# Kernel tuning notes

Hardware: AMD Instinct MI355X
Metric: run time of the kernel (lower is better)

Reference implementation:

```python
import jax, jax.numpy as jnp
import numpy as np

VOCAB = 23      # prime -> all nonzero scales invertible mod VOCAB
LEN = 256
BATCH = 512
HIDDEN = 4096
TEMP = 0.1


def _inv_table(v):
    # multiplicative inverse table mod v; inv(0) := 0 (non-invertible element)
    return np.array([0] + [pow(a, -1, v) for a in range(1, v)], dtype=np.int32)


def st_one_hot_argmax(x, temperature):
    """Straight-through one-hot argmax with tempered-softmax gradient."""
    soft = jax.nn.softmax(x / temperature, axis=-1)
    hard = jax.nn.one_hot(jnp.argmax(x, axis=-1), x.shape[-1], dtype=x.dtype)
    return soft + jax.lax.stop_gradient(hard - soft)


def one_hot_minus(inputs, shift):
    """(inputs - shift) % V in one-hot space via circular convolution."""
    V = inputs.shape[-1]
    # shift_matrix[..., u, v] = shift[..., (v - u) % V]  (== roll(shift, u))
    idx = (jnp.arange(V)[None, :] - jnp.arange(V)[:, None]) % V  # [u, v]
    shift_matrix = shift[..., idx]                               # [..., u, v]
    return jnp.einsum('...v,...uv->...u', inputs, shift_matrix)


def one_hot_multiply(inputs, scale):
    """(inputs * scale) % V in one-hot space; scale=0 component is dropped."""
    V = inputs.shape[-1]
    perm = (jnp.arange(V)[:, None] * jnp.arange(V)[None, :]) % V  # [a, v]
    P = jax.nn.one_hot(perm, V, dtype=inputs.dtype)               # [a, v, u]
    scale0 = scale * (jnp.arange(V) != 0).astype(scale.dtype)     # zero a=0 row
    return jnp.einsum('...v,...a,avu->...u', inputs, scale0, P)


def multiplicative_inverse(scale, v):
    """One-hot multiplicative inverse mod v via constant lookup table."""
    Inv = jax.nn.one_hot(jnp.asarray(_inv_table(v)), v, dtype=scale.dtype)  # [a, u]
    return jnp.einsum('...a,au->...u', scale, Inv)


def setup_inputs() -> dict:
    key = jax.random.key(0)
    k1, k2, k3 = jax.random.split(key, 3)
    tokens = jax.random.randint(k1, (BATCH, LEN), 0, VOCAB)
    inputs = jax.nn.one_hot(tokens, VOCAB, dtype=jnp.float32)     # [B, L, V]
    mask = (jnp.arange(LEN) % 2).astype(jnp.float32)[:, None]     # [L, 1]
    s1 = 1.0 / np.sqrt(LEN * VOCAB)
    s2 = 1.0 / np.sqrt(HIDDEN)
    W1 = jax.random.normal(k2, (LEN * VOCAB, HIDDEN), dtype=jnp.float32) * s1
    b1 = jnp.zeros((HIDDEN,), dtype=jnp.float32)
    W2 = jax.random.normal(k3, (HIDDEN, LEN * 2 * VOCAB), dtype=jnp.float32) * s2
    b2 = jnp.zeros((LEN * 2 * VOCAB,), dtype=jnp.float32)
    return {"inputs": inputs, "mask": mask, "W1": W1, "b1": b1, "W2": W2, "b2": b2}


def reference(inputs, mask, W1, b1, W2, b2):
    B, L, V = inputs.shape
    masked_inputs = mask * inputs                                 # [B, L, V]
    # layer(mask * inputs): flatten -> MLP -> [B, L, 2V]
    h = jax.nn.relu(masked_inputs.reshape(B, L * V) @ W1 + b1)
    net = (h @ W2 + b2).reshape(B, L, 2 * V)
    loc, scale = net[..., :V], net[..., V:]
    loc = st_one_hot_argmax(loc, TEMP)
    scale = st_one_hot_argmax(scale, TEMP)
    inv_scale = multiplicative_inverse(scale, V)
    shifted = one_hot_minus(inputs, loc)
    masked_outputs = (1.0 - mask) * one_hot_multiply(shifted, inv_scale)
    return masked_inputs + masked_outputs
```

## Files before the change

kernel.cpp:

```cpp
#include <hip/hip_runtime.h>
#include <cstddef>
#include <cstdint>

#define VOC 23
#define SEQ 256
#define NB  512
#define HID 4096
#define NCOL 11776
#define NPK 5888
#define KP  12288
#define EPS_TIE 4e-5f

__constant__ int INV23[VOC] = {0,1,12,8,6,14,4,10,3,18,7,21,2,16,5,20,13,19,9,17,15,11,22};

typedef __attribute__((ext_vector_type(8))) short short8;
typedef __attribute__((ext_vector_type(4))) float f32x4;

static __device__ __forceinline__ unsigned int f2bf(float f) {
  unsigned int x = __float_as_uint(f);
  return (x + 0x7fffu + ((x >> 16) & 1u)) >> 16;
}
static __device__ __forceinline__ float bf2f(unsigned int u) {
  return __uint_as_float(u << 16);
}

#define GL2LDS(g, l) __builtin_amdgcn_global_load_lds(                      \
    (const __attribute__((address_space(1))) unsigned int*)(g),             \
    (__attribute__((address_space(3))) unsigned int*)(l), 16, 0, 0)

__global__ __launch_bounds__(256) void k_tok_copy(const float* __restrict__ in,
                                                  float* __restrict__ out,
                                                  int* __restrict__ tok) {
  const int b = blockIdx.x;
  const int l = threadIdx.x;
  const float* row = in + ((size_t)b * SEQ + l) * VOC;
  int t = 0; float best = -1.0f;
#pragma unroll
  for (int v = 0; v < VOC; ++v) { float x = row[v]; if (x > best) { best = x; t = v; } }
  tok[b * SEQ + l] = t;
  if (l & 1) {
    float* o = out + ((size_t)b * SEQ + l) * VOC;
#pragma unroll
    for (int v = 0; v < VOC; ++v) o[v] = row[v];
  }
}

__global__ __launch_bounds__(256) void k_pack_w2(const float* __restrict__ W2,
                                                 unsigned short* __restrict__ Bp) {
  const int k0 = blockIdx.x * 64;
  const int j0 = blockIdx.y * 64;
  const int tid = threadIdx.x;
  __shared__ float T[64 * 65];
#pragma unroll
  for (int it = 0; it < 16; ++it) {
    int idx = it * 256 + tid;
    int k_l = idx >> 6, j_l = idx & 63;
    int j = j0 + j_l;
    int ee = j / 46, cc = j - ee * 46;
    T[j_l * 65 + k_l] = W2[(size_t)(k0 + k_l) * NCOL + 92 * ee + cc];
  }
  __syncthreads();
  const int j_l = tid >> 2, qt = tid & 3;
  unsigned int d[24];
#pragma unroll
  for (int pr = 0; pr < 8; ++pr) {
    int k_l = qt * 16 + pr * 2;
    float va = T[j_l * 65 + k_l], vb = T[j_l * 65 + k_l + 1];
    unsigned int ha = f2bf(va), la = f2bf(va - bf2f(ha));
    unsigned int hb = f2bf(vb), lb = f2bf(vb - bf2f(hb));
    d[pr * 3 + 0] = ha | (la << 16);
    d[pr * 3 + 1] = ha | (hb << 16);
    d[pr * 3 + 2] = lb | (hb << 16);
  }
  char* dst = ((char*)Bp) + (size_t)(j0 + j_l) * (KP * 2) + 6 * k0 + 96 * qt;
#pragma unroll
  for (int u = 0; u < 6; ++u) {
    uint4 w = make_uint4(d[4 * u], d[4 * u + 1], d[4 * u + 2], d[4 * u + 3]);
    ((uint4*)dst)[u] = w;
  }
}

__global__ __launch_bounds__(256) void k_hidden(const float* __restrict__ W1,
                                                const float* __restrict__ b1,
                                                const int* __restrict__ tok,
                                                float* __restrict__ h,
                                                unsigned short* __restrict__ Ap) {
  const int b = blockIdx.x;
  const int tid = threadIdx.x;
  __shared__ int rowS[128];
  if (tid < 128) {
    const int l = 2 * tid + 1;
    rowS[tid] = l * VOC + tok[b * SEQ + l];
  }
  __syncthreads();
  float4 acc[4];
#pragma unroll
  for (int j = 0; j < 4; ++j) acc[j] = make_float4(0.f, 0.f, 0.f, 0.f);
  for (int i = 0; i < 128; i += 2) {
    const float4* wr0 = (const float4*)(W1 + (size_t)rowS[i] * HID);
    const float4* wr1 = (const float4*)(W1 + (size_t)rowS[i + 1] * HID);
    float4 w0[4], w1[4];
#pragma unroll
    for (int j = 0; j < 4; ++j) w0[j] = wr0[tid + 256 * j];
#pragma unroll
    for (int j = 0; j < 4; ++j) w1[j] = wr1[tid + 256 * j];
#pragma unroll
    for (int j = 0; j < 4; ++j) {
      acc[j].x += w0[j].x; acc[j].y += w0[j].y; acc[j].z += w0[j].z; acc[j].w += w0[j].w;
      acc[j].x += w1[j].x; acc[j].y += w1[j].y; acc[j].z += w1[j].z; acc[j].w += w1[j].w;
    }
  }
  float4* hb = (float4*)(h + (size_t)b * HID);
  const float4* bv = (const float4*)b1;
#pragma unroll
  for (int j = 0; j < 4; ++j) {
    float4 bb = bv[tid + 256 * j];
    float4 r;
    r.x = fmaxf(acc[j].x + bb.x, 0.f);
    r.y = fmaxf(acc[j].y + bb.y, 0.f);
    r.z = fmaxf(acc[j].z + bb.z, 0.f);
    r.w = fmaxf(acc[j].w + bb.w, 0.f);
    hb[tid + 256 * j] = r;
    unsigned int h0 = f2bf(r.x), L0 = f2bf(r.x - bf2f(h0));
    unsigned int h1 = f2bf(r.y), L1 = f2bf(r.y - bf2f(h1));
    unsigned int h2 = f2bf(r.z), L2 = f2bf(r.z - bf2f(h2));
    unsigned int h3 = f2bf(r.w), L3 = f2bf(r.w - bf2f(h3));
    uint2* ap = (uint2*)(((char*)Ap) + (size_t)b * (KP * 2) + 24 * (tid + 256 * j));
    ap[0] = make_uint2(h0 | (h0 << 16), L0 | (h1 << 16));
    ap[1] = make_uint2(h1 | (L1 << 16), h2 | (h2 << 16));
    ap[2] = make_uint2(L2 | (h3 << 16), h3 | (L3 << 16));
  }
}

#define STAGE(bufA, bufB, kbv) do {                                               \
    _Pragma("unroll")                                                             \
    for (int c_ = 0; c_ < 2; ++c_) {                                              \
      GL2LDS(((const char*)Ap) + aG[c_] + (kbv), ((char*)(bufA)) + ldsOff[c_]);   \
      GL2LDS(((const char*)Bp) + bG[c_] + (kbv), ((char*)(bufB)) + ldsOff[c_]);   \
    }                                                                             \
  } while (0)

#define COMPUTE(bufA, bufB) do {                                                  \
    short8 a_[4], b_[4];                                                          \
    _Pragma("unroll")                                                             \
    for (int i_ = 0; i_ < 4; ++i_)                                                \
      a_[i_] = *(const short8*)((const char*)(bufA) + aoff + 1024 * i_);          \
    _Pragma("unroll")                                                             \
    for (int j_ = 0; j_ < 4; ++j_)                                                \
      b_[j_] = *(const short8*)((const char*)(bufB) + boff + 1024 * j_);          \
    _Pragma("unroll")                                                             \
    for (int i_ = 0; i_ < 4; ++i_)                                                \
      _Pragma("unroll")                                                           \
      for (int j_ = 0; j_ < 4; ++j_)                                              \
        acc[i_][j_] = __builtin_amdgcn_mfma_f32_16x16x32_bf16(a_[i_], b_[j_],     \
                                                              acc[i_][j_], 0, 0, 0); \
  } while (0)

__global__ __launch_bounds__(256) void k3_mfma(const unsigned short* __restrict__ Ap,
                                               const unsigned short* __restrict__ Bp,
                                               float* __restrict__ partial) {
  __shared__ unsigned short AsmD[2][128 * 32];
  __shared__ unsigned short BsmD[2][128 * 32];
  const int tid = threadIdx.x;

  const int f = blockIdx.x;
  const int nf = (f & 7) * 92 + (f >> 3);
  const int bn0 = (nf >> 4) * 128;
  const int inner = nf & 15;
  const int bm0 = (inner & 3) * 128;
  const int s = inner >> 2;

  const int lane = tid & 63, wave = tid >> 6;
  const int wm = wave & 1, wn = wave >> 1;
  const int r = lane & 15, q = lane >> 4;

  size_t aG[2], bG[2]; int ldsOff[2];
#pragma unroll
  for (int c = 0; c < 2; ++c) {
    const int G = c * 256 + tid;
    const int line = G >> 3, gph = G & 7;
    const int gin = gph ^ (line & 7);
    const int grow = 2 * line + (gin >> 2);
    const int gcol = (gin & 3) << 4;
    aG[c] = (size_t)(bm0 + grow) * (KP * 2) + gcol;
    bG[c] = (size_t)(bn0 + grow) * (KP * 2) + gcol;
    ldsOff[c] = G * 16;
  }

  const int gphR = (((((r & 1) << 2) | q) ^ ((r >> 1) & 7)) << 4);
  const int aoff = (32 * wm + (r >> 1)) * 128 + gphR;
  const int boff = (32 * wn + (r >> 1)) * 128 + gphR;

  f32x4 acc[4][4];
#pragma unroll
  for (int i = 0; i < 4; ++i)
#pragma unroll
    for (int j = 0; j < 4; ++j) acc[i][j] = (f32x4){0.f, 0.f, 0.f, 0.f};

  const int kb0 = s * 6144;
  STAGE(AsmD[0], BsmD[0], kb0);
  __syncthreads();
#pragma unroll 1
  for (int it = 0; it < 96; it += 2) {
    const int kb = kb0 + it * 64;
    STAGE(AsmD[1], BsmD[1], kb + 64);
    COMPUTE(AsmD[0], BsmD[0]);
    __syncthreads();
    if (it < 94) STAGE(AsmD[0], BsmD[0], kb + 128);
    COMPUTE(AsmD[1], BsmD[1]);
    __syncthreads();
  }

  float* pbase = partial + (size_t)s * NB * NPK;
#pragma unroll
  for (int i = 0; i < 4; ++i) {
    const int m = bm0 + 64 * wm + 16 * i + 4 * q;
#pragma unroll
    for (int j = 0; j < 4; ++j) {
      const int n = bn0 + 64 * wn + 16 * j + r;
      float* pp = pbase + (size_t)m * NPK + n;
#pragma unroll
      for (int reg = 0; reg < 4; ++reg)
        pp[(size_t)reg * NPK] = acc[i][j][reg];
    }
  }
}

__global__ __launch_bounds__(256) void k_epilogue(const float* __restrict__ partial,
                                                  const float* __restrict__ b2,
                                                  const int* __restrict__ tok,
                                                  int* __restrict__ win,
                                                  int* __restrict__ gcnt,
                                                  int* __restrict__ glist,
                                                  float* __restrict__ out) {
  const int b = blockIdx.x, tid = threadIdx.x;
  const int e = tid >> 1, grp = tid & 1;
  __shared__ int winS[256];
  __shared__ int flagS[256];
  float x[VOC];
  const size_t base = (size_t)b * NPK + 46 * e + 23 * grp;
#pragma unroll
  for (int c = 0; c < VOC; ++c) x[c] = b2[92 * e + 23 * grp + c];
#pragma unroll
  for (int s2 = 0; s2 < 4; ++s2) {
    const float* pp = partial + (size_t)s2 * NB * NPK + base;
#pragma unroll
    for (int c = 0; c < VOC; ++c) x[c] += pp[c];
  }
  float b0 = -1e30f, b1v = -1e30f; int bi = 0;
#pragma unroll
  for (int c = 0; c < VOC; ++c) {
    if (x[c] > b0) { b1v = b0; b0 = x[c]; bi = c; }
    else if (x[c] > b1v) b1v = x[c];
  }
  winS[tid] = bi;
  flagS[tid] = (b0 - b1v < EPS_TIE) ? 1 : 0;
  __syncthreads();
  if (!grp) {
    const int loc = winS[tid], sc = winS[tid + 1];
    win[b * 256 + 2 * e] = loc;
    win[b * 256 + 2 * e + 1] = sc;
    const int f0 = flagS[tid], f1 = flagS[tid + 1];
    if (f0 | f1) {
      int idx = atomicAdd(gcnt, 1);
      glist[idx] = e | (b << 7) | (f0 << 16) | (f1 << 17);
    }
    const int l = 2 * e;
    float* o = out + ((size_t)b * SEQ + l) * VOC;
    if (sc == 0) {
      for (int v = 0; v < VOC; ++v) o[v] = 0.f;
    } else {
      const int t = tok[b * SEQ + l];
      int dd = t - loc; if (dd < 0) dd += VOC;
      const int u = (INV23[sc] * dd) % VOC;
      for (int v = 0; v < VOC; ++v) o[v] = (v == u) ? 1.f : 0.f;
    }
  }
}

__global__ __launch_bounds__(192) void k_recheck(const float* __restrict__ h,
                                                 const float* __restrict__ W2,
                                                 const float* __restrict__ b2,
                                                 const int* __restrict__ tok,
                                                 const int* __restrict__ win,
                                                 const int* __restrict__ gcnt,
                                                 const int* __restrict__ glist,
                                                 float* __restrict__ out) {
  const int tid = threadIdx.x;
  __shared__ double dpart[184];
  __shared__ double dlog[VOC];
  __shared__ int decS[2];
  const int n = gcnt[0];
  for (int ei = blockIdx.x; ei < n; ei += 128) {
    const int ent = glist[ei];
    const int e = ent & 127, b = (ent >> 7) & 511;
    const int l = 2 * e;
#pragma unroll
    for (int grp = 0; grp < 2; ++grp) {
      if (!(ent & (1 << (16 + grp)))) {
        if (tid == 0) decS[grp] = win[b * 256 + 2 * e + grp];
      } else {
        const int col0 = 92 * e + 23 * grp;
        if (tid < 184) {
          const int c = tid >> 3, part = tid & 7;
          const float* hb = h + (size_t)b * HID;
          const size_t colc = (size_t)(col0 + c);
          double sacc[8] = {0, 0, 0, 0, 0, 0, 0, 0};
          const int kbase = part * 512;
          for (int kk = 0; kk < 512; kk += 8) {
#pragma unroll
            for (int t2 = 0; t2 < 8; ++t2) {
              const int k = kbase + kk + t2;
              sacc[t2] += (double)hb[k] * (double)W2[(size_t)k * NCOL + colc];
            }
          }
          dpart[tid] = ((sacc[0] + sacc[1]) + (sacc[2] + sacc[3])) +
                       ((sacc[4] + sacc[5]) + (sacc[6] + sacc[7]));
        }
        __syncthreads();
        if (tid < VOC) {
          double sd = (double)b2[col0 + tid];
#pragma unroll
          for (int p2 = 0; p2 < 8; ++p2) sd += dpart[tid * 8 + p2];
          dlog[tid] = sd;
        }
        __syncthreads();
        if (tid == 0) {
          double best = -1e300; int bi2 = 0;
#pragma unroll
          for (int c = 0; c < VOC; ++c)
            if (dlog[c] > best) { best = dlog[c]; bi2 = c; }
          decS[grp] = bi2;
        }
      }
      __syncthreads();
    }
    if (tid < VOC) {
      const int loc = decS[0], sc = decS[1];
      float val = 0.f;
      if (sc != 0) {
        const int t = tok[b * SEQ + l];
        int dd = t - loc; if (dd < 0) dd += VOC;
        const int u = (INV23[sc] * dd) % VOC;
        val = (tid == u) ? 1.f : 0.f;
      }
      out[((size_t)b * SEQ + l) * VOC + tid] = val;
    }
    __syncthreads();
  }
}

extern "C" void kernel_launch(void* const* d_in, const int* in_sizes, int n_in,
                              void* d_out, int out_size, void* d_ws, size_t ws_size,
                              hipStream_t stream) {
  const float* in  = (const float*)d_in[0];
  const float* W1  = (const float*)d_in[2];
  const float* b1  = (const float*)d_in[3];
  const float* W2  = (const float*)d_in[4];
  const float* b2  = (const float*)d_in[5];
  float* out = (float*)d_out;

  char* w = (char*)d_ws;
  int* tok = (int*)w;                         w += (size_t)NB * SEQ * 4;
  float* h = (float*)w;                       w += (size_t)NB * HID * 4;
  unsigned short* Ap = (unsigned short*)w;    w += (size_t)NB * KP * 2;
  unsigned short* Bp = (unsigned short*)w;    w += (size_t)NPK * KP * 2;
  float* partial = (float*)w;                 w += (size_t)4 * NB * NPK * 4;
  int* win = (int*)w;                         w += (size_t)NB * 256 * 4;
  int* gcnt = (int*)w;                        w += 256;
  int* glist = (int*)w;                       w += (size_t)65536 * 4;

  k_tok_copy<<<dim3(NB), dim3(256), 0, stream>>>(in, out, tok);
  k_pack_w2<<<dim3(64, 92), dim3(256), 0, stream>>>(W2, Bp);
  k_hidden<<<dim3(NB), dim3(256), 0, stream>>>(W1, b1, tok, h, Ap);
  hipMemsetAsync(gcnt, 0, 4, stream);
  k3_mfma<<<dim3(736), dim3(256), 0, stream>>>(Ap, Bp, partial);
  k_epilogue<<<dim3(NB), dim3(256), 0, stream>>>(partial, b2, tok, win, gcnt, glist, out);
  k_recheck<<<dim3(128), dim3(192), 0, stream>>>(h, W2, b2, tok, win, gcnt, glist, out);
}
```

Baseline: 699.8 us.

## Enlarge GEMM tiles to 256x256 with a 4-slot LDS async-load pipeline

Rewrites the main bf16 MFMA GEMM so each 512-thread block computes a 256x256 tile (8x4 MFMA fragments per wave) instead of 128x128. The K loop now streams into a 4-slot LDS ring buffer with three stages in flight, gated by explicit vmcnt waits and a single barrier per step. The setprio hint is raised around the MFMA bursts. The aim is more data reuse per LDS load and better hiding of global-memory latency. The cost is higher register pressure, 128KB of LDS per block, and only 184 blocks, which may underfill the CUs.

```diff
diff --git a/kernel.cpp b/kernel.cpp
--- a/kernel.cpp
+++ b/kernel.cpp
@@ -132,98 +132,132 @@
   }
 }
 
-#define STAGE(bufA, bufB, kbv) do {                                               \
+__global__ __launch_bounds__(512, 2) void k3_mfma(const unsigned short* __restrict__ Ap,
+                                                  const unsigned short* __restrict__ Bp,
+                                                  float* __restrict__ partial) {
+  __shared__ char lds3[4 * 32768];
+  const int tid = threadIdx.x;
+
+  const int f = blockIdx.x;
+  const int d = (f & 7) * 23 + (f >> 3);
+  const int g = d >> 1, mi = d & 1;
+  const int s = g / 23, n = g - s * 23;
+  const int bm0 = mi * 256;
+  const int bn0 = n * 256;
+  const int kb0 = s * 6144;
+
+  const int lane = tid & 63, wave = tid >> 6;
+  const int wm = wave & 1, wn = wave >> 1;
+  const int r = lane & 15, q = lane >> 4;
+
+  size_t gsrc[4]; int gdst[4];
+#pragma unroll
+  for (int c = 0; c < 4; ++c) {
+    const int G = (c & 1) * 512 + tid;
+    const int line = G >> 3, gph = G & 7;
+    const int gin = gph ^ (line & 7);
+    const int grow = 2 * line + (gin >> 2);
+    const int gcol = (gin & 3) << 4;
+    const int row0 = (c < 2 ? bm0 : bn0) + grow;
+    gsrc[c] = (size_t)row0 * (KP * 2) + gcol;
+    gdst[c] = G * 16;
+  }
+
+#define STAGE3(slot, kbv) do {                                                    \
+    char* ldsb_ = lds3 + ((slot) << 15);                                          \
+    GL2LDS(((const char*)Ap) + gsrc[0] + (kbv), ldsb_ + gdst[0]);                 \
+    GL2LDS(((const char*)Ap) + gsrc[1] + (kbv), ldsb_ + gdst[1]);                 \
+    GL2LDS(((const char*)Bp) + gsrc[2] + (kbv), ldsb_ + 16384 + gdst[2]);         \
+    GL2LDS(((const char*)Bp) + gsrc[3] + (kbv), ldsb_ + 16384 + gdst[3]);         \
+  } while (0)
+
+  const int gphR = (((((r & 1) << 2) | q) ^ ((r >> 1) & 7)) << 4);
+  const int aoff = (wm * 64 + (r >> 1)) * 128 + gphR;
+  const int boff = (wn * 32 + (r >> 1)) * 128 + gphR;
+
+  f32x4 acc[8][4];
+#pragma unroll
+  for (int i = 0; i < 8; ++i)
+#pragma unroll
+    for (int j = 0; j < 4; ++j) acc[i][j] = (f32x4){0.f, 0.f, 0.f, 0.f};
+
+#define COMPUTE3(slot) do {                                                       \
+    const char* sb_ = lds3 + ((slot) << 15);                                      \
+    short8 a_[8], b_[4];                                                          \
     _Pragma("unroll")                                                             \
-    for (int c_ = 0; c_ < 2; ++c_) {                                              \
-      GL2LDS(((const char*)Ap) + aG[c_] + (kbv), ((char*)(bufA)) + ldsOff[c_]);   \
-      GL2LDS(((const char*)Bp) + bG[c_] + (kbv), ((char*)(bufB)) + ldsOff[c_]);   \
-    }                                                                             \
-  } while (0)
-
-#define COMPUTE(bufA, bufB) do {                                                  \
-    short8 a_[4], b_[4];                                                          \
-    _Pragma("unroll")                                                             \
-    for (int i_ = 0; i_ < 4; ++i_)                                                \
-      a_[i_] = *(const short8*)((const char*)(bufA) + aoff + 1024 * i_);          \
+    for (int i_ = 0; i_ < 8; ++i_)                                                \
+      a_[i_] = *(const short8*)(sb_ + aoff + i_ * 1024);                          \
     _Pragma("unroll")                                                             \
     for (int j_ = 0; j_ < 4; ++j_)                                                \
-      b_[j_] = *(const short8*)((const char*)(bufB) + boff + 1024 * j_);          \
+      b_[j_] = *(const short8*)(sb_ + 16384 + boff + j_ * 1024);                  \
+    __builtin_amdgcn_s_setprio(1);                                                \
     _Pragma("unroll")                                                             \
-    for (int i_ = 0; i_ < 4; ++i_)                                                \
+    for (int i_ = 0; i_ < 8; ++i_)                                                \
       _Pragma("unroll")                                                           \
       for (int j_ = 0; j_ < 4; ++j_)                                              \
         acc[i_][j_] = __builtin_amdgcn_mfma_f32_16x16x32_bf16(a_[i_], b_[j_],     \
                                                               acc[i_][j_], 0, 0, 0); \
+    __builtin_amdgcn_s_setprio(0);                                                \
   } while (0)
 
-__global__ __launch_bounds__(256) void k3_mfma(const unsigned short* __restrict__ Ap,
-                                               const unsigned short* __restrict__ Bp,
-                                               float* __restrict__ partial) {
-  __shared__ unsigned short AsmD[2][128 * 32];
-  __shared__ unsigned short BsmD[2][128 * 32];
-  const int tid = threadIdx.x;
-
-  const int f = blockIdx.x;
-  const int nf = (f & 7) * 92 + (f >> 3);
-  const int bn0 = (nf >> 4) * 128;
-  const int inner = nf & 15;
-  const int bm0 = (inner & 3) * 128;
-  const int s = inner >> 2;
-
-  const int lane = tid & 63, wave = tid >> 6;
-  const int wm = wave & 1, wn = wave >> 1;
-  const int r = lane & 15, q = lane >> 4;
-
-  size_t aG[2], bG[2]; int ldsOff[2];
-#pragma unroll
-  for (int c = 0; c < 2; ++c) {
-    const int G = c * 256 + tid;
-    const int line = G >> 3, gph = G & 7;
-    const int gin = gph ^ (line & 7);
-    const int grow = 2 * line + (gin >> 2);
-    const int gcol = (gin & 3) << 4;
-    aG[c] = (size_t)(bm0 + grow) * (KP * 2) + gcol;
-    bG[c] = (size_t)(bn0 + grow) * (KP * 2) + gcol;
-    ldsOff[c] = G * 16;
-  }
-
-  const int gphR = (((((r & 1) << 2) | q) ^ ((r >> 1) & 7)) << 4);
-  const int aoff = (32 * wm + (r >> 1)) * 128 + gphR;
-  const int boff = (32 * wn + (r >> 1)) * 128 + gphR;
-
-  f32x4 acc[4][4];
-#pragma unroll
-  for (int i = 0; i < 4; ++i)
-#pragma unroll
-    for (int j = 0; j < 4; ++j) acc[i][j] = (f32x4){0.f, 0.f, 0.f, 0.f};
-
-  const int kb0 = s * 6144;
-  STAGE(AsmD[0], BsmD[0], kb0);
-  __syncthreads();
+  STAGE3(0, kb0);
+  STAGE3(1, kb0 + 64);
+  STAGE3(2, kb0 + 128);
+
 #pragma unroll 1
-  for (int it = 0; it < 96; it += 2) {
-    const int kb = kb0 + it * 64;
-    STAGE(AsmD[1], BsmD[1], kb + 64);
-    COMPUTE(AsmD[0], BsmD[0]);
-    __syncthreads();
-    if (it < 94) STAGE(AsmD[0], BsmD[0], kb + 128);
-    COMPUTE(AsmD[1], BsmD[1]);
-    __syncthreads();
-  }
+  for (int t = 0; t < 93; ++t) {
+    asm volatile("s_waitcnt vmcnt(8)" ::: "memory");
+    __builtin_amdgcn_s_barrier();
+    __builtin_amdgcn_sched_barrier(0);
+    const int slot = t & 3;
+    {
+      const char* sb_ = lds3 + (slot << 15);
+      short8 a_[8], b_[4];
+#pragma unroll
+      for (int i_ = 0; i_ < 8; ++i_)
+        a_[i_] = *(const short8*)(sb_ + aoff + i_ * 1024);
+#pragma unroll
+      for (int j_ = 0; j_ < 4; ++j_)
+        b_[j_] = *(const short8*)(sb_ + 16384 + boff + j_ * 1024);
+      STAGE3((t + 3) & 3, kb0 + (t + 3) * 64);
+      __builtin_amdgcn_s_setprio(1);
+#pragma unroll
+      for (int i_ = 0; i_ < 8; ++i_)
+#pragma unroll
+        for (int j_ = 0; j_ < 4; ++j_)
+          acc[i_][j_] = __builtin_amdgcn_mfma_f32_16x16x32_bf16(a_[i_], b_[j_],
+                                                                acc[i_][j_], 0, 0, 0);
+      __builtin_amdgcn_s_setprio(0);
+    }
+  }
+  asm volatile("s_waitcnt vmcnt(8)" ::: "memory");
+  __builtin_amdgcn_s_barrier();
+  __builtin_amdgcn_sched_barrier(0);
+  COMPUTE3(93 & 3);
+  asm volatile("s_waitcnt vmcnt(4)" ::: "memory");
+  __builtin_amdgcn_s_barrier();
+  __builtin_amdgcn_sched_barrier(0);
+  COMPUTE3(94 & 3);
+  asm volatile("s_waitcnt vmcnt(0)" ::: "memory");
+  __builtin_amdgcn_s_barrier();
+  __builtin_amdgcn_sched_barrier(0);
+  COMPUTE3(95 & 3);
 
   float* pbase = partial + (size_t)s * NB * NPK;
 #pragma unroll
-  for (int i = 0; i < 4; ++i) {
-    const int m = bm0 + 64 * wm + 16 * i + 4 * q;
+  for (int i = 0; i < 8; ++i) {
+    const int m = bm0 + wm * 128 + 16 * i + 4 * q;
 #pragma unroll
     for (int j = 0; j < 4; ++j) {
-      const int n = bn0 + 64 * wn + 16 * j + r;
-      float* pp = pbase + (size_t)m * NPK + n;
+      const int nn = bn0 + wn * 64 + 16 * j + r;
+      float* pp = pbase + (size_t)m * NPK + nn;
 #pragma unroll
       for (int reg = 0; reg < 4; ++reg)
         pp[(size_t)reg * NPK] = acc[i][j][reg];
     }
   }
+#undef STAGE3
+#undef COMPUTE3
 }
 
 __global__ __launch_bounds__(256) void k_epilogue(const float* __restrict__ partial,
@@ -374,7 +408,7 @@
   k_pack_w2<<<dim3(64, 92), dim3(256), 0, stream>>>(W2, Bp);
   k_hidden<<<dim3(NB), dim3(256), 0, stream>>>(W1, b1, tok, h, Ap);
   hipMemsetAsync(gcnt, 0, 4, stream);
-  k3_mfma<<<dim3(736), dim3(256), 0, stream>>>(Ap, Bp, partial);
+  k3_mfma<<<dim3(184), dim3(512), 0, stream>>>(Ap, Bp, partial);
   k_epilogue<<<dim3(NB), dim3(256), 0, stream>>>(partial, b2, tok, win, gcnt, glist, out);
   k_recheck<<<dim3(128), dim3(192), 0, stream>>>(h, W2, b2, tok, win, gcnt, glist, out);
 }
```

Result: faster. 621.9 us (-11.1%).
